# Kernel tuning notes

Measured on AMD Instinct MI355X. Metric: run time of the kernel, lower is better.

Reference implementation:

```python
import jax, jax.numpy as jnp
import numpy as np

B, N, M, F = 64, 2048, 2048, 4   # batch, n_pred_points, n_gt_points, feature cols
D = 2                            # loss_indices = [0, 1] -> (x, y) coords


def setup_inputs() -> dict:
    key = jax.random.key(0)
    k1, k2 = jax.random.split(key)
    preds = jax.random.normal(k1, (B, N, F), dtype=jnp.float32)
    targs = jax.random.normal(k2, (B, M, F), dtype=jnp.float32)
    subcoef = jnp.ones((D,), dtype=jnp.float32)
    return {"preds": preds, "targs": targs, "subcoef": subcoef}


def _bidirectional_nn_loss(p, t, subcoef):
    # p: [B, N, D] pred coords, t: [B, M, D] gt coords
    # squared euclidean pairwise distances [B, N, M]
    d2 = (jnp.sum(p * p, axis=-1)[:, :, None]
          + jnp.sum(t * t, axis=-1)[:, None, :]
          - 2.0 * jnp.einsum('bnd,bmd->bnm', p, t))
    # gt_tree: nearest gt for every pred point
    nn_gt = jnp.argmin(d2, axis=2)    # [B, N]
    # pred_tree: nearest pred for every gt point
    nn_pr = jnp.argmin(d2, axis=1)    # [B, M]
    t_nn = jnp.take_along_axis(t, nn_gt[:, :, None], axis=1)  # [B, N, D]
    p_nn = jnp.take_along_axis(p, nn_pr[:, :, None], axis=1)  # [B, M, D]
    move_preds_to_gt = jnp.sum(jnp.abs(p - t_nn) * subcoef)   # subcoef only on this term
    move_gts_to_pred = jnp.sum(jnp.abs(p_nn - t))
    return move_preds_to_gt + move_gts_to_pred


def reference(preds, targs, subcoef):
    p = preds[..., :D]   # loss_indices = [0, 1]
    t = targs[..., :D]
    return _bidirectional_nn_loss(p, t, subcoef)
```

## Files before the change

kernel.cpp:

```cpp
#include <hip/hip_runtime.h>

constexpr int B = 64;
constexpr int N = 2048;
constexpr int M = 2048;
constexpr int F = 4;
constexpr int BLOCK = 256;
constexpr int P = 2;
constexpr int CHUNK = 16;
constexpr int NCHUNK = M / CHUNK;
constexpr int CH_F4 = 9;
constexpr unsigned DMASK = 0xFFFFF800u;

typedef float v2f __attribute__((ext_vector_type(2)));

__device__ __forceinline__ unsigned fbits(float x) {
    union { float f; unsigned u; } c; c.f = x; return c.u;
}
__device__ __forceinline__ float min3f(float a, float b, float c) {
    float r;
    asm("v_min3_f32 %0, %1, %2, %3" : "=v"(r) : "v"(a), "v"(b), "v"(c));
    return r;
}
__device__ __forceinline__ v2f pk_mul(v2f a, v2f b) {
    v2f d;
    asm("v_pk_mul_f32 %0, %1, %2" : "=v"(d) : "v"(a), "v"(b));
    return d;
}
__device__ __forceinline__ v2f pk_add(v2f a, v2f b) {
    v2f d;
    asm("v_pk_add_f32 %0, %1, %2" : "=v"(d) : "v"(a), "v"(b));
    return d;
}
__device__ __forceinline__ v2f pk_fma(v2f a, v2f b, v2f c) {
    v2f d;
    asm("v_pk_fma_f32 %0, %1, %2, %3" : "=v"(d) : "v"(a), "v"(b), "v"(c));
    return d;
}

__global__ void __launch_bounds__(BLOCK)
nn_kernel(const float* __restrict__ preds,
          const float* __restrict__ targs,
          const float* __restrict__ subcoef,
          float* __restrict__ out) {
    __shared__ float4 sc4[NCHUNK * CH_F4];
    __shared__ float  wsum[BLOCK / 64];

    const int dir = blockIdx.z;
    const int b   = blockIdx.y;
    const int tid = threadIdx.x;

    const float* src = dir ? targs : preds;
    const float* dst = dir ? preds : targs;

    const float* dstb = dst + (size_t)b * M * F;
    for (int g = tid; g < M / 2; g += BLOCK) {
        const float4 a = *reinterpret_cast<const float4*>(dstb + (size_t)(2 * g) * F);
        const float4 c = *reinterpret_cast<const float4*>(dstb + (size_t)(2 * g + 1) * F);
        sc4[(g >> 3) * CH_F4 + (g & 7)] = make_float4(a.x, c.x, a.y, c.y);
    }
    __syncthreads();

    const int base = blockIdx.x * (BLOCK * P);
    float px[P], py[P], p2s[P];
    v2f n2x[P], n2y[P], p2v[P];
    unsigned bkey[P];
    #pragma unroll
    for (int j = 0; j < P; ++j) {
        const int n = base + j * BLOCK + tid;
        const float2 p = *reinterpret_cast<const float2*>(src + ((size_t)b * N + n) * F);
        px[j] = p.x;  py[j] = p.y;
        p2s[j] = fmaf(p.y, p.y, p.x * p.x);
        const float ax = -2.0f * p.x, ay = -2.0f * p.y;
        n2x[j] = (v2f){ ax, ax };
        n2y[j] = (v2f){ ay, ay };
        p2v[j] = (v2f){ p2s[j], p2s[j] };
        bkey[j] = 0xFFFFFFFFu;
    }

    #pragma unroll 2
    for (int c = 0; c < NCHUNK; ++c) {
        const float4* chp = sc4 + c * CH_F4;
        float cb[P];
        #pragma unroll
        for (int j = 0; j < P; ++j) cb[j] = 3.4028235e38f;
        #pragma unroll
        for (int i = 0; i < CHUNK / 2; ++i) {
            const float4 q = chp[i];
            const v2f XX = { q.x, q.y };
            const v2f YY = { q.z, q.w };
            const v2f NN = pk_fma(YY, YY, pk_mul(XX, XX));
            #pragma unroll
            for (int j = 0; j < P; ++j) {
                v2f d = pk_fma(XX, n2x[j], pk_add(NN, p2v[j]));
                d = pk_fma(YY, n2y[j], d);
                cb[j] = min3f(d.x, d.y, cb[j]);
            }
        }
        #pragma unroll
        for (int j = 0; j < P; ++j) {
            const unsigned key = (fbits(cb[j]) & DMASK) | (unsigned)c;
            bkey[j] = key < bkey[j] ? key : bkey[j];
        }
    }

    float c0 = 1.0f, c1 = 1.0f;
    if (dir == 0) { c0 = subcoef[0]; c1 = subcoef[1]; }
    float acc = 0.0f;
    #pragma unroll
    for (int j = 0; j < P; ++j) {
        const int cwin = (int)(bkey[j] & 0x7FFu);
        const unsigned dbits = bkey[j] & DMASK;
        const float a2x = -2.0f * px[j];
        const float a2y = -2.0f * py[j];
        const float4* chp = sc4 + cwin * CH_F4;
        int iwin = 0x7FFFFFFF;
        #pragma unroll
        for (int i = 0; i < CHUNK / 2; ++i) {
            const float4 q = chp[i];
            float dA = fmaf(q.z, q.z, q.x * q.x);
            dA = fmaf(q.x, a2x, dA + p2s[j]);
            dA = fmaf(q.z, a2y, dA);
            const bool hA = (fbits(dA) & DMASK) == dbits;
            iwin = (hA && 2 * i < iwin) ? 2 * i : iwin;
            float dB = fmaf(q.w, q.w, q.y * q.y);
            dB = fmaf(q.y, a2x, dB + p2s[j]);
            dB = fmaf(q.w, a2y, dB);
            const bool hB = (fbits(dB) & DMASK) == dbits;
            iwin = (hB && 2 * i + 1 < iwin) ? 2 * i + 1 : iwin;
        }
        if (iwin == 0x7FFFFFFF) iwin = 0;
        const float4 qq = chp[iwin >> 1];
        const float qx = (iwin & 1) ? qq.y : qq.x;
        const float qy = (iwin & 1) ? qq.w : qq.z;
        acc += fabsf(px[j] - qx) * c0 + fabsf(py[j] - qy) * c1;
    }

    #pragma unroll
    for (int off = 32; off > 0; off >>= 1) acc += __shfl_down(acc, off, 64);
    if ((tid & 63) == 0) wsum[tid >> 6] = acc;
    __syncthreads();
    if (tid == 0) {
        float s = 0.0f;
        #pragma unroll
        for (int w = 0; w < BLOCK / 64; ++w) s += wsum[w];
        atomicAdd(out, s);
    }
}

extern "C" void kernel_launch(void* const* d_in, const int* in_sizes, int n_in,
                              void* d_out, int out_size, void* d_ws, size_t ws_size,
                              hipStream_t stream) {
    const float* preds   = (const float*)d_in[0];
    const float* targs   = (const float*)d_in[1];
    const float* subcoef = (const float*)d_in[2];
    float* out = (float*)d_out;

    hipMemsetAsync(out, 0, sizeof(float), stream);

    dim3 grid(N / (BLOCK * P), B, 2);
    nn_kernel<<<grid, BLOCK, 0, stream>>>(preds, targs, subcoef, out);
}
```

Baseline: 124.7 us.

## Split candidate set across blocks with workspace keys and separate combine kernel

Each nearest-neighbor search is split into two kernels. The scan kernel handles all queries of a batch but only a slice of the candidate chunks, and writes packed distance/chunk-index keys to workspace. A combine kernel takes the min over slices, rescans the winning chunk from global memory and accumulates the loss. The query norm is dropped from the distances in favour of a constant bias, and the key mask is narrowed to 7 index bits. This cuts shared-memory staging per block and puts more queries per thread, at the cost of an extra launch, workspace traffic and coarser distance keys that could mis-pick near ties.

```diff
diff --git a/kernel.cpp b/kernel.cpp
--- a/kernel.cpp
+++ b/kernel.cpp
@@ -1,15 +1,17 @@
 #include <hip/hip_runtime.h>
 
 constexpr int B = 64;
-constexpr int N = 2048;
+constexpr int NQ = 2048;
 constexpr int M = 2048;
 constexpr int F = 4;
 constexpr int BLOCK = 256;
-constexpr int P = 2;
+constexpr int P = 8;
 constexpr int CHUNK = 16;
 constexpr int NCHUNK = M / CHUNK;
 constexpr int CH_F4 = 9;
-constexpr unsigned DMASK = 0xFFFFF800u;
+constexpr unsigned DMASK = 0xFFFFFF80u;
+constexpr float BIAS = 64.0f;
+constexpr int QTOT = 2 * B * NQ;
 
 typedef float v2f __attribute__((ext_vector_type(2)));
 
@@ -22,36 +24,156 @@
     return r;
 }
 __device__ __forceinline__ v2f pk_mul(v2f a, v2f b) {
-    v2f d;
-    asm("v_pk_mul_f32 %0, %1, %2" : "=v"(d) : "v"(a), "v"(b));
-    return d;
+    v2f d; asm("v_pk_mul_f32 %0, %1, %2" : "=v"(d) : "v"(a), "v"(b)); return d;
 }
 __device__ __forceinline__ v2f pk_add(v2f a, v2f b) {
-    v2f d;
-    asm("v_pk_add_f32 %0, %1, %2" : "=v"(d) : "v"(a), "v"(b));
-    return d;
+    v2f d; asm("v_pk_add_f32 %0, %1, %2" : "=v"(d) : "v"(a), "v"(b)); return d;
 }
 __device__ __forceinline__ v2f pk_fma(v2f a, v2f b, v2f c) {
-    v2f d;
-    asm("v_pk_fma_f32 %0, %1, %2, %3" : "=v"(d) : "v"(a), "v"(b), "v"(c));
-    return d;
-}
-
+    v2f d; asm("v_pk_fma_f32 %0, %1, %2, %3" : "=v"(d) : "v"(a), "v"(b), "v"(c)); return d;
+}
+
+template <int S>
 __global__ void __launch_bounds__(BLOCK)
-nn_kernel(const float* __restrict__ preds,
-          const float* __restrict__ targs,
-          const float* __restrict__ subcoef,
-          float* __restrict__ out) {
+nn_scan(const float* __restrict__ preds,
+        const float* __restrict__ targs,
+        unsigned* __restrict__ keys,
+        float* __restrict__ out) {
+    constexpr int CPB = NCHUNK / S;
+    __shared__ float4 sc4[CPB * CH_F4];
+
+    const int s   = blockIdx.x;
+    const int b   = blockIdx.y;
+    const int dir = blockIdx.z;
+    const int tid = threadIdx.x;
+
+    if (s == 0 && b == 0 && dir == 0 && tid == 0) *out = 0.0f;
+
+    const float* qsrc = dir ? targs : preds;
+    const float* csrc = dir ? preds : targs;
+
+    const float* cb_ = csrc + ((size_t)b * M + (size_t)s * CPB * CHUNK) * F;
+    for (int g = tid; g < CPB * 8; g += BLOCK) {
+        const float4 a = *reinterpret_cast<const float4*>(cb_ + (size_t)(2 * g) * F);
+        const float4 c = *reinterpret_cast<const float4*>(cb_ + (size_t)(2 * g + 1) * F);
+        sc4[(g >> 3) * CH_F4 + (g & 7)] = make_float4(a.x, c.x, a.y, c.y);
+    }
+    __syncthreads();
+
+    v2f n2x[P], n2y[P];
+    unsigned bkey[P];
+    #pragma unroll
+    for (int j = 0; j < P; ++j) {
+        const int n = j * BLOCK + tid;
+        const float2 p = *reinterpret_cast<const float2*>(qsrc + ((size_t)b * NQ + n) * F);
+        const float ax = -2.0f * p.x, ay = -2.0f * p.y;
+        n2x[j] = (v2f){ ax, ax };
+        n2y[j] = (v2f){ ay, ay };
+        bkey[j] = 0xFFFFFFFFu;
+    }
+    const v2f biasv = (v2f){ BIAS, BIAS };
+
+    for (int c = 0; c < CPB; ++c) {
+        const float4* chp = sc4 + c * CH_F4;
+        float cbm[P];
+        #pragma unroll
+        for (int j = 0; j < P; ++j) cbm[j] = 3.4028235e38f;
+        #pragma unroll
+        for (int i = 0; i < CHUNK / 2; ++i) {
+            const float4 q = chp[i];
+            const v2f XX = { q.x, q.y };
+            const v2f YY = { q.z, q.w };
+            const v2f NN = pk_add(pk_fma(YY, YY, pk_mul(XX, XX)), biasv);
+            #pragma unroll
+            for (int j = 0; j < P; ++j) {
+                v2f d = pk_fma(XX, n2x[j], NN);
+                d = pk_fma(YY, n2y[j], d);
+                cbm[j] = min3f(d.x, d.y, cbm[j]);
+            }
+        }
+        const unsigned gc = (unsigned)(s * CPB + c);
+        #pragma unroll
+        for (int j = 0; j < P; ++j) {
+            const unsigned key = (fbits(cbm[j]) & DMASK) | gc;
+            bkey[j] = key < bkey[j] ? key : bkey[j];
+        }
+    }
+
+    unsigned* kout = keys + (size_t)s * QTOT + ((size_t)dir * B + b) * NQ;
+    #pragma unroll
+    for (int j = 0; j < P; ++j) kout[j * BLOCK + tid] = bkey[j];
+}
+
+__global__ void __launch_bounds__(BLOCK)
+nn_combine(const float* __restrict__ preds,
+           const float* __restrict__ targs,
+           const float* __restrict__ subcoef,
+           const unsigned* __restrict__ keys, int nsplit,
+           float* __restrict__ out) {
+    __shared__ float wsum[BLOCK / 64];
+    const int qid = blockIdx.x * BLOCK + threadIdx.x;
+    const int dir = qid >> 17;
+    const int b   = (qid >> 11) & 63;
+    const int n   = qid & 2047;
+
+    unsigned k = 0xFFFFFFFFu;
+    for (int s = 0; s < nsplit; ++s) {
+        const unsigned ks = keys[(size_t)s * QTOT + qid];
+        k = ks < k ? ks : k;
+    }
+    const int cwin = (int)(k & 0x7Fu);
+    const unsigned dbits = k & DMASK;
+
+    const float* qsrc = dir ? targs : preds;
+    const float* csrc = dir ? preds : targs;
+    const float2 p = *reinterpret_cast<const float2*>(qsrc + ((size_t)b * NQ + n) * F);
+    const float ax = -2.0f * p.x, ay = -2.0f * p.y;
+
+    const float4* cand = reinterpret_cast<const float4*>(
+        csrc + ((size_t)b * M + (size_t)cwin * CHUNK) * F);
+    float qx = 0.0f, qy = 0.0f;
+    int found = 0;
+    #pragma unroll 4
+    for (int i = 0; i < CHUNK; ++i) {
+        const float4 t4 = cand[i];
+        const float x = t4.x, y = t4.y;
+        float d = fmaf(y, y, x * x) + BIAS;
+        d = fmaf(x, ax, d);
+        d = fmaf(y, ay, d);
+        const bool hit = (((fbits(d) & DMASK) == dbits) && !found);
+        qx = hit ? x : qx;
+        qy = hit ? y : qy;
+        found = hit ? 1 : found;
+    }
+    if (!found) { qx = cand[0].x; qy = cand[0].y; }
+
+    float c0 = 1.0f, c1 = 1.0f;
+    if (dir == 0) { c0 = subcoef[0]; c1 = subcoef[1]; }
+    float acc = fabsf(p.x - qx) * c0 + fabsf(p.y - qy) * c1;
+
+    #pragma unroll
+    for (int off = 32; off > 0; off >>= 1) acc += __shfl_down(acc, off, 64);
+    if ((threadIdx.x & 63) == 0) wsum[threadIdx.x >> 6] = acc;
+    __syncthreads();
+    if (threadIdx.x == 0) {
+        float ssum = 0.0f;
+        #pragma unroll
+        for (int w = 0; w < BLOCK / 64; ++w) ssum += wsum[w];
+        atomicAdd(out, ssum);
+    }
+}
+
+constexpr int PF = 2;
+__global__ void __launch_bounds__(BLOCK)
+nn_fallback(const float* __restrict__ preds,
+            const float* __restrict__ targs,
+            const float* __restrict__ subcoef,
+            float* __restrict__ out) {
     __shared__ float4 sc4[NCHUNK * CH_F4];
     __shared__ float  wsum[BLOCK / 64];
-
-    const int dir = blockIdx.z;
-    const int b   = blockIdx.y;
-    const int tid = threadIdx.x;
-
+    const int dir = blockIdx.z, b = blockIdx.y, tid = threadIdx.x;
     const float* src = dir ? targs : preds;
     const float* dst = dir ? preds : targs;
-
     const float* dstb = dst + (size_t)b * M * F;
     for (int g = tid; g < M / 2; g += BLOCK) {
         const float4 a = *reinterpret_cast<const float4*>(dstb + (size_t)(2 * g) * F);
@@ -59,91 +181,77 @@
         sc4[(g >> 3) * CH_F4 + (g & 7)] = make_float4(a.x, c.x, a.y, c.y);
     }
     __syncthreads();
-
-    const int base = blockIdx.x * (BLOCK * P);
-    float px[P], py[P], p2s[P];
-    v2f n2x[P], n2y[P], p2v[P];
-    unsigned bkey[P];
-    #pragma unroll
-    for (int j = 0; j < P; ++j) {
+    const int base = blockIdx.x * (BLOCK * PF);
+    float px[PF], py[PF];
+    v2f n2x[PF], n2y[PF];
+    unsigned bkey[PF];
+    #pragma unroll
+    for (int j = 0; j < PF; ++j) {
         const int n = base + j * BLOCK + tid;
-        const float2 p = *reinterpret_cast<const float2*>(src + ((size_t)b * N + n) * F);
-        px[j] = p.x;  py[j] = p.y;
-        p2s[j] = fmaf(p.y, p.y, p.x * p.x);
-        const float ax = -2.0f * p.x, ay = -2.0f * p.y;
-        n2x[j] = (v2f){ ax, ax };
-        n2y[j] = (v2f){ ay, ay };
-        p2v[j] = (v2f){ p2s[j], p2s[j] };
+        const float2 p = *reinterpret_cast<const float2*>(src + ((size_t)b * NQ + n) * F);
+        px[j] = p.x; py[j] = p.y;
+        n2x[j] = (v2f){ -2.0f * p.x, -2.0f * p.x };
+        n2y[j] = (v2f){ -2.0f * p.y, -2.0f * p.y };
         bkey[j] = 0xFFFFFFFFu;
     }
-
-    #pragma unroll 2
+    const v2f biasv = (v2f){ BIAS, BIAS };
     for (int c = 0; c < NCHUNK; ++c) {
         const float4* chp = sc4 + c * CH_F4;
-        float cb[P];
-        #pragma unroll
-        for (int j = 0; j < P; ++j) cb[j] = 3.4028235e38f;
+        float cbm[PF];
+        #pragma unroll
+        for (int j = 0; j < PF; ++j) cbm[j] = 3.4028235e38f;
         #pragma unroll
         for (int i = 0; i < CHUNK / 2; ++i) {
             const float4 q = chp[i];
             const v2f XX = { q.x, q.y };
             const v2f YY = { q.z, q.w };
-            const v2f NN = pk_fma(YY, YY, pk_mul(XX, XX));
+            const v2f NN = pk_add(pk_fma(YY, YY, pk_mul(XX, XX)), biasv);
             #pragma unroll
-            for (int j = 0; j < P; ++j) {
-                v2f d = pk_fma(XX, n2x[j], pk_add(NN, p2v[j]));
+            for (int j = 0; j < PF; ++j) {
+                v2f d = pk_fma(XX, n2x[j], NN);
                 d = pk_fma(YY, n2y[j], d);
-                cb[j] = min3f(d.x, d.y, cb[j]);
+                cbm[j] = min3f(d.x, d.y, cbm[j]);
             }
         }
         #pragma unroll
-        for (int j = 0; j < P; ++j) {
-            const unsigned key = (fbits(cb[j]) & DMASK) | (unsigned)c;
+        for (int j = 0; j < PF; ++j) {
+            const unsigned key = (fbits(cbm[j]) & DMASK) | (unsigned)c;
             bkey[j] = key < bkey[j] ? key : bkey[j];
         }
     }
-
     float c0 = 1.0f, c1 = 1.0f;
     if (dir == 0) { c0 = subcoef[0]; c1 = subcoef[1]; }
     float acc = 0.0f;
     #pragma unroll
-    for (int j = 0; j < P; ++j) {
-        const int cwin = (int)(bkey[j] & 0x7FFu);
+    for (int j = 0; j < PF; ++j) {
+        const int cwin = (int)(bkey[j] & 0x7Fu);
         const unsigned dbits = bkey[j] & DMASK;
-        const float a2x = -2.0f * px[j];
-        const float a2y = -2.0f * py[j];
+        const float a2x = -2.0f * px[j], a2y = -2.0f * py[j];
         const float4* chp = sc4 + cwin * CH_F4;
-        int iwin = 0x7FFFFFFF;
+        float qx = 0.0f, qy = 0.0f; int found = 0;
         #pragma unroll
         for (int i = 0; i < CHUNK / 2; ++i) {
             const float4 q = chp[i];
-            float dA = fmaf(q.z, q.z, q.x * q.x);
-            dA = fmaf(q.x, a2x, dA + p2s[j]);
-            dA = fmaf(q.z, a2y, dA);
-            const bool hA = (fbits(dA) & DMASK) == dbits;
-            iwin = (hA && 2 * i < iwin) ? 2 * i : iwin;
-            float dB = fmaf(q.w, q.w, q.y * q.y);
-            dB = fmaf(q.y, a2x, dB + p2s[j]);
-            dB = fmaf(q.w, a2y, dB);
-            const bool hB = (fbits(dB) & DMASK) == dbits;
-            iwin = (hB && 2 * i + 1 < iwin) ? 2 * i + 1 : iwin;
-        }
-        if (iwin == 0x7FFFFFFF) iwin = 0;
-        const float4 qq = chp[iwin >> 1];
-        const float qx = (iwin & 1) ? qq.y : qq.x;
-        const float qy = (iwin & 1) ? qq.w : qq.z;
+            float dA = fmaf(q.z, q.z, q.x * q.x) + BIAS;
+            dA = fmaf(q.x, a2x, dA); dA = fmaf(q.z, a2y, dA);
+            bool hit = (((fbits(dA) & DMASK) == dbits) && !found);
+            qx = hit ? q.x : qx; qy = hit ? q.z : qy; found = hit ? 1 : found;
+            float dB = fmaf(q.w, q.w, q.y * q.y) + BIAS;
+            dB = fmaf(q.y, a2x, dB); dB = fmaf(q.w, a2y, dB);
+            hit = (((fbits(dB) & DMASK) == dbits) && !found);
+            qx = hit ? q.y : qx; qy = hit ? q.w : qy; found = hit ? 1 : found;
+        }
         acc += fabsf(px[j] - qx) * c0 + fabsf(py[j] - qy) * c1;
     }
-
     #pragma unroll
     for (int off = 32; off > 0; off >>= 1) acc += __shfl_down(acc, off, 64);
     if ((tid & 63) == 0) wsum[tid >> 6] = acc;
     __syncthreads();
     if (tid == 0) {
-        float s = 0.0f;
-        #pragma unroll
-        for (int w = 0; w < BLOCK / 64; ++w) s += wsum[w];
-        atomicAdd(out, s);
+        float ssum = 0.0f;
+        #pragma unroll
+        for (int w = 0; w < BLOCK / 64; ++w) ssum += wsum[w];
+        atomicAdd(out, ssum);
     }
 }
 
@@ -155,8 +263,21 @@
     const float* subcoef = (const float*)d_in[2];
     float* out = (float*)d_out;
 
-    hipMemsetAsync(out, 0, sizeof(float), stream);
-
-    dim3 grid(N / (BLOCK * P), B, 2);
-    nn_kernel<<<grid, BLOCK, 0, stream>>>(preds, targs, subcoef, out);
-}
+    const size_t need8 = (size_t)8 * QTOT * sizeof(unsigned);
+    const size_t need4 = (size_t)4 * QTOT * sizeof(unsigned);
+    const size_t need2 = (size_t)2 * QTOT * sizeof(unsigned);
+
+    if (d_ws != nullptr && ws_size >= need2) {
+        unsigned* keys = (unsigned*)d_ws;
+        int S;
+        if (ws_size >= need8)      { S = 8; nn_scan<8><<<dim3(8, B, 2), BLOCK, 0, stream>>>(preds, targs, keys, out); }
+        else if (ws_size >= need4) { S = 4; nn_scan<4><<<dim3(4, B, 2), BLOCK, 0, stream>>>(preds, targs, keys, out); }
+        else                       { S = 2; nn_scan<2><<<dim3(2, B, 2), BLOCK, 0, stream>>>(preds, targs, keys, out); }
+        nn_combine<<<dim3(QTOT / BLOCK), BLOCK, 0, stream>>>(
+            preds, targs, subcoef, keys, S, out);
+    } else {
+        hipMemsetAsync(out, 0, sizeof(float), stream);
+        dim3 grid(NQ / (BLOCK * PF), B, 2);
+        nn_fallback<<<grid, BLOCK, 0, stream>>>(preds, targs, subcoef, out);
+    }
+}
```

Result: faster. 114.9 us (-7.8%).
